# Kernel tuning notes

Hardware: AMD Instinct MI355X
Metric: run time of the kernel (lower is better)

## Reference

```python
import jax, jax.numpy as jnp
import numpy as np
from jax import lax

BETA = 0.9   # membrane decay
THR = 1.0    # firing threshold (soft reset)
K = 10       # number of time bins
# spatial pyramid for original_shape=(100,368) under 4 stride-2 SAME convs
HW = [(50, 184), (25, 92), (13, 46), (7, 23)]
CH = [4, 8, 16, 32]


def conv(x, w, b, stride=1):
    y = lax.conv_general_dilated(x, w, (stride, stride), 'SAME',
                                 dimension_numbers=('NCHW', 'OIHW', 'NCHW'))
    return y + b[None, :, None, None]


def spike(u):
    # heaviside forward, sigmoid straight-through surrogate backward
    s = (u > 0.0).astype(u.dtype)
    sg = jax.nn.sigmoid(4.0 * u)
    return sg + lax.stop_gradient(s - sg)


def setup_inputs() -> dict:
    key = jax.random.key(0)
    ks = jax.random.split(key, 12)
    T, B = 1000, 1
    x = jax.random.normal(ks[0], (T, B, 1, 100, 368), jnp.float32)

    def w(k, o, i, kh=3, kw=3):
        return 0.1 * jax.random.normal(k, (o, i, kh, kw), jnp.float32)

    inp = {'x': x}
    cin = [1] + CH[:3]
    for li in range(4):
        inp['w%d' % (li + 1)] = w(ks[1 + li], CH[li], cin[li])
        inp['b%d' % (li + 1)] = jnp.zeros((CH[li],), jnp.float32)
    sc = [2 * K * c for c in CH]  # skip channels: [80,160,320,640]
    inp['dw4'] = w(ks[5], 64, sc[3]); inp['db4'] = jnp.zeros((64,), jnp.float32)
    inp['dw3'] = w(ks[6], 32, 64 + sc[2]); inp['db3'] = jnp.zeros((32,), jnp.float32)
    inp['dw2'] = w(ks[7], 16, 32 + sc[1]); inp['db2'] = jnp.zeros((16,), jnp.float32)
    inp['dw1'] = w(ks[8], 8, 16 + sc[0]); inp['db1'] = jnp.zeros((8,), jnp.float32)
    inp['wo'] = w(ks[9], 1, 8, 1, 1); inp['bo'] = jnp.zeros((1,), jnp.float32)
    inp['total_steps'] = 1000
    inp['block_size'] = 100
    return inp


def reference(x, w1, b1, w2, b2, w3, b3, w4, b4,
              dw4, db4, dw3, db3, dw2, db2, dw1, db1, wo, bo,
              total_steps, block_size):
    S = total_steps // K  # steps per bin
    B = x.shape[1]
    xb = x.reshape((K, S) + x.shape[1:])  # [K,S,B,C,H,W]
    mems0 = tuple(jnp.zeros((B, CH[i], HW[i][0], HW[i][1]), x.dtype) for i in range(4))
    enc_w = [(w1, b1), (w2, b2), (w3, b3), (w4, b4)]

    def forward_step(x_t, mems):
        new_mems, spk = [], x_t
        for (wi, bi), m in zip(enc_w, mems):
            m = BETA * m + conv(spk, wi, bi, 2)
            spk = spike(m - THR)
            m = m - spk * THR  # soft reset
            new_mems.append(m)
        return tuple(new_mems)

    def step(carry, x_t):
        mems, sums, sqs = carry
        mems = forward_step(x_t, mems)
        sums = tuple(s + m for s, m in zip(sums, mems))
        sqs = tuple(q + m * m for q, m in zip(sqs, mems))
        return (mems, sums, sqs), None

    def bin_fn(mems, x_bin):
        zeros = tuple(jnp.zeros_like(m) for m in mems)
        (mems, sums, sqs), _ = lax.scan(step, (mems, zeros, zeros), x_bin)
        means = tuple(s / S for s in sums)
        stds = tuple(jnp.sqrt(jnp.maximum(q / S - mu * mu, 1e-8))
                     for q, mu in zip(sqs, means))
        return mems, (means, stds)

    _, (means, stds) = lax.scan(bin_fn, mems0, xb)  # each leaf: [K,B,C,H,W]

    def skip(mean, std):
        # torch.cat([mean0,std0,mean1,std1,...], dim=1) channel ordering
        f = jnp.stack([mean, std], axis=1)        # [K,2,B,C,H,W]
        f = jnp.transpose(f, (2, 0, 1, 3, 4, 5))  # [B,K,2,C,H,W]
        b_, k_, t_, c_, h_, w_ = f.shape
        return f.reshape(b_, k_ * t_ * c_, h_, w_)

    skips = [skip(means[i], stds[i]) for i in range(4)]

    def up(t, hw):
        return jax.image.resize(t, (t.shape[0], t.shape[1], hw[0], hw[1]), 'bilinear')

    relu = jax.nn.relu
    d = relu(conv(skips[3], dw4, db4))
    d = relu(conv(jnp.concatenate([up(d, HW[2]), skips[2]], 1), dw3, db3))
    d = relu(conv(jnp.concatenate([up(d, HW[1]), skips[1]], 1), dw2, db2))
    d = relu(conv(jnp.concatenate([up(d, HW[0]), skips[0]], 1), dw1, db1))
    tau_c = conv(up(d, (100, 368)), wo, bo)  # [B,1,100,368]
    return tau_c
```

## Files before the change

### kernel.cpp

```cpp
#include <hip/hip_runtime.h>

#define KBINS  10
#define SBIN   100
#define BETA   0.9f
#define THR    1.0f
#define CDIV(a,b) (((a)+(b)-1)/(b))


__global__ void k_zero16(float4* __restrict__ p, int n16) {
    int i = blockIdx.x * blockDim.x + threadIdx.x;
    if (i < n16) p[i] = make_float4(0.f, 0.f, 0.f, 0.f);
}

__global__ void k_conv1(const float* __restrict__ x,
                        const float* __restrict__ w1,
                        const float* __restrict__ b1,
                        float* __restrict__ c1) {
    int n = blockIdx.x * blockDim.x + threadIdx.x;
    if (n >= 1000 * 50 * 46) return;
    int wq  = n % 46;
    int tmp = n / 46;
    int h   = tmp % 50;
    int t   = tmp / 50;
    int w0  = wq * 4;

    const float* xt = x + (size_t)t * 36800;
    float rm2 = (h  < 49)  ? 1.f : 0.f;
    float cm8 = (w0 < 180) ? 1.f : 0.f;
    int   r2  = min(2 * h + 2, 99);
    int   cb  = 2 * w0;
    int   c8  = min(cb + 8, 367);

    const float* row0 = xt + (2 * h) * 368 + cb;
    const float* row1 = row0 + 368;
    const float* row2 = xt + r2 * 368 + cb;

    float tap[3][9];
    #pragma unroll
    for (int j = 0; j < 8; j++) {
        tap[0][j] = row0[j];
        tap[1][j] = row1[j];
        tap[2][j] = row2[j] * rm2;
    }
    tap[0][8] = xt[(2 * h) * 368 + c8] * cm8;
    tap[1][8] = xt[(2 * h + 1) * 368 + c8] * cm8;
    tap[2][8] = xt[r2 * 368 + c8] * (rm2 * cm8);

    float* ot = c1 + (size_t)t * 36800 + h * 184 + w0;
    #pragma unroll
    for (int co = 0; co < 4; co++) {
        float b = b1[co];
        float a0 = b, a1 = b, a2 = b, a3 = b;
        #pragma unroll
        for (int r = 0; r < 3; r++) {
            #pragma unroll
            for (int kw = 0; kw < 3; kw++) {
                float wv = w1[co * 9 + r * 3 + kw];
                a0 = fmaf(tap[r][0 + kw], wv, a0);
                a1 = fmaf(tap[r][2 + kw], wv, a1);
                a2 = fmaf(tap[r][4 + kw], wv, a2);
                a3 = fmaf(tap[r][6 + kw], wv, a3);
            }
        }
        *(float4*)(ot + (size_t)co * 9200) = make_float4(a0, a1, a2, a3);
    }
}

__global__ void k_scan(const float* __restrict__ cbuf,
                       unsigned char* __restrict__ spk,
                       float* __restrict__ skip,
                       float* __restrict__ mscratch,
                       int C, int HW, int Win, int Wp, int HpWp, int write_spk) {
    const int PF = 20;
    int CHW = C * HW;
    int p = blockIdx.x * blockDim.x + threadIdx.x;
    if (p >= CHW) return;
    int c  = p / HW;
    int hw = p - c * HW;
    int h  = hw / Win, w = hw - h * Win;

    const size_t tstr = (size_t)C * HpWp;
    unsigned char* sp = spk + (size_t)c * HpWp + (h + 1) * Wp + (w + 1);

    float m = 0.0f;
    float va[PF], vb[PF];
    #pragma unroll
    for (int j = 0; j < PF; j++) va[j] = cbuf[(size_t)j * CHW + p];

    const int T = KBINS * SBIN;
    for (int k = 0; k < KBINS; k++) {
        float s = 0.0f, q = 0.0f;
        for (int b = 0; b < SBIN / PF; b++) {
            int t0 = k * SBIN + b * PF;
            int tn = t0 + PF;
            bool more = (tn < T);
            #pragma unroll
            for (int j = 0; j < PF; j++)
                vb[j] = more ? cbuf[(size_t)(tn + j) * CHW + p] : 0.0f;
            #pragma unroll
            for (int j = 0; j < PF; j++) {
                m = fmaf(m, BETA, va[j]);
                float spv = (m - THR > 0.0f) ? 1.0f : 0.0f;
                m -= spv * THR;
                if (write_spk) sp[(size_t)(t0 + j) * tstr] = (unsigned char)spv;
                s += m;
                q = fmaf(m, m, q);
            }
            #pragma unroll
            for (int j = 0; j < PF; j++) va[j] = vb[j];
        }
        float mean = s * (1.0f / SBIN);
        float var  = q * (1.0f / SBIN) - mean * mean;
        float sd   = sqrtf(fmaxf(var, 1e-8f));
        skip[(size_t)(k * 2 * C + c) * HW + hw]     = mean;
        skip[(size_t)(k * 2 * C + C + c) * HW + hw] = sd;
    }
    mscratch[p] = m;
}

template<int CIN, int COUT, int COG, int OW,
         int HOUT, int WOUT, int PADH, int HP, int WP>
__global__ void k_convs2(const unsigned char* __restrict__ spk,
                         const float* __restrict__ wt,
                         const float* __restrict__ bias,
                         float* __restrict__ out) {
    const int WQ = (WOUT + OW - 1) / OW;
    const int NT = 2 * OW + 1;
    int n = blockIdx.x * blockDim.x + threadIdx.x;
    if (n >= 1000 * HOUT * WQ) return;
    int wq  = n % WQ;
    int tmp = n / WQ;
    int h   = tmp % HOUT;
    int t   = tmp / HOUT;
    int cog = blockIdx.y;
    int w0  = wq * OW;

    const unsigned char* base = spk + (size_t)t * CIN * HP * WP
                              + (2 * h - PADH + 1) * WP + (2 * w0 + 1);

    float acc[OW][COG];
    #pragma unroll
    for (int q = 0; q < OW; q++)
        #pragma unroll
        for (int co = 0; co < COG; co++) acc[q][co] = bias[cog * COG + co];

    for (int ci = 0; ci < CIN; ci++) {
        const unsigned char* ic = base + (size_t)ci * HP * WP;
        float tap[3][NT];
        #pragma unroll
        for (int r = 0; r < 3; r++)
            #pragma unroll
            for (int j = 0; j < NT; j++)
                tap[r][j] = (float)ic[r * WP + j];
        #pragma unroll
        for (int co = 0; co < COG; co++) {
            const float* wc = wt + ((size_t)(cog * COG + co) * CIN + ci) * 9;
            #pragma unroll
            for (int r = 0; r < 3; r++)
                #pragma unroll
                for (int kw = 0; kw < 3; kw++) {
                    float wv = wc[r * 3 + kw];
                    #pragma unroll
                    for (int q = 0; q < OW; q++)
                        acc[q][co] = fmaf(tap[r][2 * q + kw], wv, acc[q][co]);
                }
        }
    }

    float* ot = out + ((size_t)t * COUT + cog * COG) * (HOUT * WOUT) + h * WOUT + w0;
    #pragma unroll
    for (int co = 0; co < COG; co++) {
        float* oc = ot + (size_t)co * (HOUT * WOUT);
        if constexpr (OW == 4) {
            *(float4*)oc = make_float4(acc[0][co], acc[1][co], acc[2][co], acc[3][co]);
        } else {
            if (w0 + 2 <= WOUT) *(float2*)oc = make_float2(acc[0][co], acc[1][co]);
            else                oc[0] = acc[0][co];
        }
    }
}

__global__ void k_up_cat(const float* __restrict__ up_src, int Cup, int Hi, int Wi,
                         const float* __restrict__ skip, int Cskip,
                         float* __restrict__ out, int Ho, int Wo) {
    int total = (Cup + Cskip) * Ho * Wo;
    int n = blockIdx.x * blockDim.x + threadIdx.x;
    if (n >= total) return;
    int w   = n % Wo;
    int tmp = n / Wo;
    int h   = tmp % Ho;
    int c   = tmp / Ho;
    float v;
    if (c < Cup) {
        float ph = (h + 0.5f) * (float)Hi / (float)Ho - 0.5f;
        float pw = (w + 0.5f) * (float)Wi / (float)Wo - 0.5f;
        float fh = floorf(ph), fw = floorf(pw);
        int h0 = (int)fh, w0 = (int)fw;
        float ah = ph - fh, aw = pw - fw;
        int h0c = min(max(h0, 0), Hi - 1), h1c = min(max(h0 + 1, 0), Hi - 1);
        int w0c = min(max(w0, 0), Wi - 1), w1c = min(max(w0 + 1, 0), Wi - 1);
        const float* sc = up_src + (size_t)c * Hi * Wi;
        float v00 = sc[h0c * Wi + w0c], v01 = sc[h0c * Wi + w1c];
        float v10 = sc[h1c * Wi + w0c], v11 = sc[h1c * Wi + w1c];
        v = (1.0f - ah) * ((1.0f - aw) * v00 + aw * v01)
          + ah * ((1.0f - aw) * v10 + aw * v11);
    } else {
        v = skip[(size_t)(c - Cup) * Ho * Wo + h * Wo + w];
    }
    out[n] = v;
}

template<int CIN, int CS, int COG>
__global__ void k_dconv(const float* __restrict__ in,
                        const float* __restrict__ wt,
                        float* __restrict__ part,
                        int Cout, int H, int W) {
    int HW  = H * W;
    int pix = blockIdx.x * blockDim.x + threadIdx.x;
    if (pix >= HW) return;
    int co0   = blockIdx.y * COG;
    int chunk = blockIdx.z;
    int h = pix / W, w = pix - h * W;

    int off[9]; float msk[9];
    #pragma unroll
    for (int kh = 0; kh < 3; kh++) {
        int r = h + kh - 1;
        bool rok = (r >= 0) && (r < H);
        int rc = rok ? r : 0;
        #pragma unroll
        for (int kw = 0; kw < 3; kw++) {
            int cc = w + kw - 1;
            bool cok = (cc >= 0) && (cc < W);
            int ccc = cok ? cc : 0;
            off[kh * 3 + kw] = rc * W + ccc;
            msk[kh * 3 + kw] = (rok && cok) ? 1.0f : 0.0f;
        }
    }

    const float* ibase = in + (size_t)chunk * CS * HW;
    const float* wbase = wt + ((size_t)co0 * CIN + (size_t)chunk * CS) * 9;

    float acc[COG];
    #pragma unroll
    for (int co = 0; co < COG; co++) acc[co] = 0.0f;

    #pragma unroll 8
    for (int ci = 0; ci < CS; ci++) {
        const float* ic = ibase + (size_t)ci * HW;
        float tap[9];
        #pragma unroll
        for (int j = 0; j < 9; j++)
            tap[j] = msk[j] * ic[off[j]];
        #pragma unroll
        for (int co = 0; co < COG; co++) {
            const float* wc = wbase + ((size_t)co * CIN + ci) * 9;
            #pragma unroll
            for (int j = 0; j < 9; j++)
                acc[co] = fmaf(tap[j], wc[j], acc[co]);
        }
    }

    float* pp = part + ((size_t)chunk * Cout + co0) * HW + pix;
    #pragma unroll
    for (int co = 0; co < COG; co++) pp[(size_t)co * HW] = acc[co];
}

__global__ void k_reduce_relu(const float* __restrict__ part,
                              const float* __restrict__ bias,
                              float* __restrict__ out,
                              int Cout, int HW, int nchunks) {
    int n = blockIdx.x * blockDim.x + threadIdx.x;
    if (n >= Cout * HW) return;
    int co = n / HW;
    float acc = bias[co];
    for (int c = 0; c < nchunks; c++)
        acc += part[(size_t)c * Cout * HW + n];
    out[n] = fmaxf(acc, 0.0f);
}

__global__ void k_final(const float* __restrict__ d1,
                        const float* __restrict__ wo,
                        const float* __restrict__ bo,
                        float* __restrict__ out) {
    int n = blockIdx.x * blockDim.x + threadIdx.x;
    if (n >= 36800) return;
    int w = n % 368, h = n / 368;
    float ph = (h + 0.5f) * 0.5f - 0.5f;
    float pw = (w + 0.5f) * 0.5f - 0.5f;
    float fh = floorf(ph), fw = floorf(pw);
    int h0 = (int)fh, w0 = (int)fw;
    float ah = ph - fh, aw = pw - fw;
    int h0c = min(max(h0, 0), 49),  h1c = min(max(h0 + 1, 0), 49);
    int w0c = min(max(w0, 0), 183), w1c = min(max(w0 + 1, 0), 183);
    float acc = bo[0];
    #pragma unroll
    for (int c = 0; c < 8; c++) {
        const float* sc = d1 + c * 9200;
        float v00 = sc[h0c * 184 + w0c], v01 = sc[h0c * 184 + w1c];
        float v10 = sc[h1c * 184 + w0c], v11 = sc[h1c * 184 + w1c];
        float v = (1.0f - ah) * ((1.0f - aw) * v00 + aw * v01)
                + ah * ((1.0f - aw) * v10 + aw * v11);
        acc = fmaf(wo[c], v, acc);
    }
    out[n] = acc;
}

extern "C" void kernel_launch(void* const* d_in, const int* in_sizes, int n_in,
                              void* d_out, int out_size, void* d_ws, size_t ws_size,
                              hipStream_t stream) {
    (void)in_sizes; (void)n_in; (void)out_size; (void)ws_size;
    const float* x   = (const float*)d_in[0];
    const float* w1  = (const float*)d_in[1];
    const float* b1  = (const float*)d_in[2];
    const float* w2  = (const float*)d_in[3];
    const float* b2  = (const float*)d_in[4];
    const float* w3  = (const float*)d_in[5];
    const float* b3  = (const float*)d_in[6];
    const float* w4  = (const float*)d_in[7];
    const float* b4  = (const float*)d_in[8];
    const float* dw4 = (const float*)d_in[9];
    const float* db4 = (const float*)d_in[10];
    const float* dw3 = (const float*)d_in[11];
    const float* db3 = (const float*)d_in[12];
    const float* dw2 = (const float*)d_in[13];
    const float* db2 = (const float*)d_in[14];
    const float* dw1 = (const float*)d_in[15];
    const float* db1 = (const float*)d_in[16];
    const float* wo  = (const float*)d_in[17];
    const float* bo  = (const float*)d_in[18];
    float* out = (float*)d_out;

    char* ws = (char*)d_ws;
    size_t off = 0;
    auto alloc = [&](size_t bytes) -> void* {
        void* p = ws + off;
        off += (bytes + 255) & ~(size_t)255;
        return p;
    };
    float*         cbuf  = (float*)alloc(147200000);
    unsigned char* spk1p = (unsigned char*)alloc(39936000);
    unsigned char* spk2p = (unsigned char*)alloc(21600000);
    unsigned char* spk3p = (unsigned char*)alloc(12960000);
    float*         skip0 = (float*)alloc(2944000);
    float*         skip1 = (float*)alloc(1472000);
    float*         skip2 = (float*)alloc(765440);
    float*         skip3 = (float*)alloc(412160);
    float*         msS   = (float*)alloc(147200);
    char* dec = (char*)cbuf;
    size_t doff = 0;
    auto dalloc = [&](size_t bytes) -> void* {
        void* p = dec + doff;
        doff += (bytes + 255) & ~(size_t)255;
        return p;
    };
    float* d4   = (float*)dalloc(10304u * 4);
    float* d3   = (float*)dalloc(19136u * 4);
    float* d2   = (float*)dalloc(36800u * 4);
    float* d1   = (float*)dalloc(73600u * 4);
    float* cat3 = (float*)dalloc(229632u * 4);
    float* cat2 = (float*)dalloc(441600u * 4);
    float* cat1 = (float*)dalloc(883200u * 4);
    float* part = (float*)dalloc(230400u * 4);

    const int BS  = 256;
    const int SBS = 64;

    {
        size_t nb = 39936000ull + 21600000 + 12960000;
        int n16 = (int)(nb / 16);
        k_zero16<<<CDIV(n16, BS), BS, 0, stream>>>((float4*)spk1p, n16);
    }

    k_conv1<<<CDIV(1000 * 50 * 46, BS), BS, 0, stream>>>(x, w1, b1, cbuf);
    k_scan<<<CDIV(36800, SBS), SBS, 0, stream>>>(cbuf, spk1p, skip0, msS,
                                                 4, 9200, 184, 192, 52 * 192, 1);

    k_convs2<4, 8, 8, 4, 25, 92, 0, 52, 192>
        <<<dim3(CDIV(1000 * 25 * 23, BS), 1), BS, 0, stream>>>(spk1p, w2, b2, cbuf);
    k_scan<<<CDIV(18400, SBS), SBS, 0, stream>>>(cbuf, spk2p, skip1, msS,
                                                 8, 2300, 92, 100, 27 * 100, 1);

    k_convs2<8, 16, 16, 2, 13, 46, 1, 27, 100>
        <<<dim3(CDIV(1000 * 13 * 23, BS), 1), BS, 0, stream>>>(spk2p, w3, b3, cbuf);
    k_scan<<<CDIV(9568, SBS), SBS, 0, stream>>>(cbuf, spk3p, skip2, msS,
                                                16, 598, 46, 54, 15 * 54, 1);

    k_convs2<16, 32, 16, 2, 7, 23, 1, 15, 54>
        <<<dim3(CDIV(1000 * 7 * 12, BS), 2), BS, 0, stream>>>(spk3p, w4, b4, cbuf);
    k_scan<<<CDIV(5152, SBS), SBS, 0, stream>>>(cbuf, spk1p , skip3, msS,
                                                32, 161, 23, 31, 9 * 31, 0);

    {
        dim3 g(CDIV(161, 64), 16, 20);
        k_dconv<640, 32, 4><<<g, 64, 0, stream>>>(skip3, dw4, part, 64, 7, 23);
        k_reduce_relu<<<CDIV(64 * 161, BS), BS, 0, stream>>>(part, db4, d4, 64, 161, 20);
    }
    {
        k_up_cat<<<CDIV(384 * 598, BS), BS, 0, stream>>>(d4, 64, 7, 23,
                                                         skip2, 320, cat3, 13, 46);
        dim3 g(CDIV(598, 64), 8, 12);
        k_dconv<384, 32, 4><<<g, 64, 0, stream>>>(cat3, dw3, part, 32, 13, 46);
        k_reduce_relu<<<CDIV(32 * 598, BS), BS, 0, stream>>>(part, db3, d3, 32, 598, 12);
    }
    {
        k_up_cat<<<CDIV(192 * 2300, BS), BS, 0, stream>>>(d3, 32, 13, 46,
                                                          skip1, 160, cat2, 25, 92);
        dim3 g(CDIV(2300, 128), 4, 6);
        k_dconv<192, 32, 4><<<g, 128, 0, stream>>>(cat2, dw2, part, 16, 25, 92);
        k_reduce_relu<<<CDIV(16 * 2300, BS), BS, 0, stream>>>(part, db2, d2, 16, 2300, 6);
    }
    {
        k_up_cat<<<CDIV(96 * 9200, BS), BS, 0, stream>>>(d2, 16, 25, 92,
                                                         skip0, 80, cat1, 50, 184);
        dim3 g(CDIV(9200, BS), 2, 3);
        k_dconv<96, 32, 4><<<g, BS, 0, stream>>>(cat1, dw1, part, 8, 50, 184);
        k_reduce_relu<<<CDIV(8 * 9200, BS), BS, 0, stream>>>(part, db1, d1, 8, 9200, 3);
    }
    k_final<<<CDIV(36800, BS), BS, 0, stream>>>(d1, wo, bo, out);
}
```

Baseline: 834.0 us.

## Chunk layer-1 conv and scan over two time halves to halve buffer

Splits the first-layer conv and membrane scan into two passes of 500 timesteps each. The membrane state carries across passes through a state buffer, and the scan gains bin-offset, bin-count and init parameters. The intent is to halve the conv output staging buffer so it is more likely to stay resident in the last-level cache, which reduces DRAM traffic between producer and scan. The spike buffers are also shifted by a 63-byte offset to change store alignment. The cost is an extra kernel launch pair and a serialization point between the two halves.

```diff
diff --git a/kernel.cpp b/kernel.cpp
--- a/kernel.cpp
+++ b/kernel.cpp
@@ -15,9 +15,9 @@
 __global__ void k_conv1(const float* __restrict__ x,
                         const float* __restrict__ w1,
                         const float* __restrict__ b1,
-                        float* __restrict__ c1) {
+                        float* __restrict__ c1, int tcount) {
     int n = blockIdx.x * blockDim.x + threadIdx.x;
-    if (n >= 1000 * 50 * 46) return;
+    if (n >= tcount * 50 * 46) return;
     int wq  = n % 46;
     int tmp = n / 46;
     int h   = tmp % 50;
@@ -69,8 +69,9 @@
 __global__ void k_scan(const float* __restrict__ cbuf,
                        unsigned char* __restrict__ spk,
                        float* __restrict__ skip,
-                       float* __restrict__ mscratch,
-                       int C, int HW, int Win, int Wp, int HpWp, int write_spk) {
+                       float* __restrict__ mstate,
+                       int C, int HW, int Win, int Wp, int HpWp,
+                       int write_spk, int bin0, int nbins, int init) {
     const int PF = 20;
     int CHW = C * HW;
     int p = blockIdx.x * blockDim.x + threadIdx.x;
@@ -80,15 +81,16 @@
     int h  = hw / Win, w = hw - h * Win;
 
     const size_t tstr = (size_t)C * HpWp;
-    unsigned char* sp = spk + (size_t)c * HpWp + (h + 1) * Wp + (w + 1);
-
-    float m = 0.0f;
+    unsigned char* sp = spk + (size_t)bin0 * SBIN * tstr
+                      + (size_t)c * HpWp + (h + 1) * Wp + (w + 1);
+
+    float m = init ? 0.0f : mstate[p];
     float va[PF], vb[PF];
     #pragma unroll
     for (int j = 0; j < PF; j++) va[j] = cbuf[(size_t)j * CHW + p];
 
-    const int T = KBINS * SBIN;
-    for (int k = 0; k < KBINS; k++) {
+    const int T = nbins * SBIN;
+    for (int k = 0; k < nbins; k++) {
         float s = 0.0f, q = 0.0f;
         for (int b = 0; b < SBIN / PF; b++) {
             int t0 = k * SBIN + b * PF;
@@ -109,13 +111,14 @@
             #pragma unroll
             for (int j = 0; j < PF; j++) va[j] = vb[j];
         }
+        int g = bin0 + k;
         float mean = s * (1.0f / SBIN);
         float var  = q * (1.0f / SBIN) - mean * mean;
         float sd   = sqrtf(fmaxf(var, 1e-8f));
-        skip[(size_t)(k * 2 * C + c) * HW + hw]     = mean;
-        skip[(size_t)(k * 2 * C + C + c) * HW + hw] = sd;
-    }
-    mscratch[p] = m;
+        skip[(size_t)(g * 2 * C + c) * HW + hw]     = mean;
+        skip[(size_t)(g * 2 * C + C + c) * HW + hw] = sd;
+    }
+    mstate[p] = m;
 }
 
 template<int CIN, int COUT, int COG, int OW,
@@ -338,15 +341,18 @@
         off += (bytes + 255) & ~(size_t)255;
         return p;
     };
-    float*         cbuf  = (float*)alloc(147200000);
-    unsigned char* spk1p = (unsigned char*)alloc(39936000);
-    unsigned char* spk2p = (unsigned char*)alloc(21600000);
-    unsigned char* spk3p = (unsigned char*)alloc(12960000);
-    float*         skip0 = (float*)alloc(2944000);
-    float*         skip1 = (float*)alloc(1472000);
-    float*         skip2 = (float*)alloc(765440);
-    float*         skip3 = (float*)alloc(412160);
-    float*         msS   = (float*)alloc(147200);
+    float* cbuf = (float*)alloc(73600000);
+    unsigned char* spk1r = (unsigned char*)alloc(39936000 + 256);
+    unsigned char* spk2r = (unsigned char*)alloc(21600000 + 256);
+    unsigned char* spk3r = (unsigned char*)alloc(12960000 + 256);
+    unsigned char* spk1p = spk1r + 63;
+    unsigned char* spk2p = spk2r + 63;
+    unsigned char* spk3p = spk3r + 63;
+    float* skip0 = (float*)alloc(2944000);
+    float* skip1 = (float*)alloc(1472000);
+    float* skip2 = (float*)alloc(765440);
+    float* skip3 = (float*)alloc(412160);
+    float* msS   = (float*)alloc(147200);
     char* dec = (char*)cbuf;
     size_t doff = 0;
     auto dalloc = [&](size_t bytes) -> void* {
@@ -367,29 +373,33 @@
     const int SBS = 64;
 
     {
-        size_t nb = 39936000ull + 21600000 + 12960000;
+        size_t nb = (39936000 + 256) + (21600000 + 256) + (12960000 + 256);
         int n16 = (int)(nb / 16);
-        k_zero16<<<CDIV(n16, BS), BS, 0, stream>>>((float4*)spk1p, n16);
-    }
-
-    k_conv1<<<CDIV(1000 * 50 * 46, BS), BS, 0, stream>>>(x, w1, b1, cbuf);
-    k_scan<<<CDIV(36800, SBS), SBS, 0, stream>>>(cbuf, spk1p, skip0, msS,
-                                                 4, 9200, 184, 192, 52 * 192, 1);
+        k_zero16<<<CDIV(n16, BS), BS, 0, stream>>>((float4*)spk1r, n16);
+    }
+
+    for (int q = 0; q < 2; q++) {
+        k_conv1<<<CDIV(500 * 50 * 46, BS), BS, 0, stream>>>(
+            x + (size_t)q * 500 * 36800, w1, b1, cbuf, 500);
+        k_scan<<<CDIV(36800, SBS), SBS, 0, stream>>>(
+            cbuf, spk1p, skip0, msS, 4, 9200, 184, 192, 52 * 192,
+            1, 5 * q, 5, (q == 0) ? 1 : 0);
+    }
 
     k_convs2<4, 8, 8, 4, 25, 92, 0, 52, 192>
         <<<dim3(CDIV(1000 * 25 * 23, BS), 1), BS, 0, stream>>>(spk1p, w2, b2, cbuf);
     k_scan<<<CDIV(18400, SBS), SBS, 0, stream>>>(cbuf, spk2p, skip1, msS,
-                                                 8, 2300, 92, 100, 27 * 100, 1);
+                                                 8, 2300, 92, 100, 27 * 100, 1, 0, 10, 1);
 
     k_convs2<8, 16, 16, 2, 13, 46, 1, 27, 100>
         <<<dim3(CDIV(1000 * 13 * 23, BS), 1), BS, 0, stream>>>(spk2p, w3, b3, cbuf);
     k_scan<<<CDIV(9568, SBS), SBS, 0, stream>>>(cbuf, spk3p, skip2, msS,
-                                                16, 598, 46, 54, 15 * 54, 1);
+                                                16, 598, 46, 54, 15 * 54, 1, 0, 10, 1);
 
     k_convs2<16, 32, 16, 2, 7, 23, 1, 15, 54>
         <<<dim3(CDIV(1000 * 7 * 12, BS), 2), BS, 0, stream>>>(spk3p, w4, b4, cbuf);
     k_scan<<<CDIV(5152, SBS), SBS, 0, stream>>>(cbuf, spk1p , skip3, msS,
-                                                32, 161, 23, 31, 9 * 31, 0);
+                                                32, 161, 23, 31, 9 * 31, 0, 0, 10, 1);
 
     {
         dim3 g(CDIV(161, 64), 16, 20);
```

Measured after the change: 837.3 us. About the same (+0.4%).
